# Performance work log

Hardware: AMD Instinct MI355X
Metric: run time of the kernel (lower is better)

Reference implementation:

```python
import jax, jax.numpy as jnp
import numpy as np

B = 256
N = 256


def setup_inputs() -> dict:
    key = jax.random.key(0)
    ks = jax.random.split(key, 6)
    X = jax.random.normal(ks[0], (B, N), dtype=jnp.float32)
    context = jax.random.normal(ks[1], (B, N), dtype=jnp.float32)
    W = jax.random.normal(ks[2], (N, N), dtype=jnp.float32) * 0.1
    scale = jnp.ones((1,), dtype=jnp.float32)
    A = jax.random.uniform(ks[3], (N, N), dtype=jnp.float32)
    cl_weight = jax.random.normal(ks[4], (N * N, N), dtype=jnp.float32) * 0.02
    cl_bias = jax.random.normal(ks[5], (N * N,), dtype=jnp.float32) * 0.02
    t = 3
    return {"X": X, "context": context, "W": W, "scale": scale, "A": A,
            "cl_weight": cl_weight, "cl_bias": cl_bias, "t": t}


def reference(X, context, W, scale, A, cl_weight, cl_bias, t):
    # context_L path: context-conditioned adjustment of W, shape [B, N, N]
    Bsz, n = X.shape
    adjust = (context @ cl_weight.T + cl_bias).reshape(Bsz, n, n)
    W_new = adjust + W  # broadcast [N,N] over batch
    # diag term: sum over rows i of (W_new @ A)[b, i, k] = einsum bij,jk->bk
    d = jnp.einsum('bij,jk->bk', W_new, A)
    eye = jnp.eye(n, dtype=X.dtype)
    L = d[:, :, None] * eye - W_new          # diag_embed(d) - W_new, [B,N,N]
    new_context = context * (t / (t + 1)) + X / (t + 1)
    L_T = scale * jnp.swapaxes(L, -1, -2)    # [B,N,N]
    update = jnp.einsum('bn,bnm->bm', X, L_T)  # matmul(X[...,None,:], L_T).squeeze()
    return (update, new_context)
```

## Files before the change

kernel.cpp:

```cpp
#include <hip/hip_runtime.h>

#define N 256
#define NN 65536

typedef __attribute__((ext_vector_type(8))) __bf16 bf16x8;
typedef __attribute__((ext_vector_type(4))) __bf16 bf16x4v;
typedef __attribute__((ext_vector_type(4))) float f32x4;

#define F_PART   0u
#define F_SPART  2097152u
#define F_WSC    2621440u
#define F_SFULL  2621696u
#define F_YADJ   2687232u
#define WS_FLOATS 2752768u

static __device__ __forceinline__ f32x4 mfma16(bf16x8 a, bf16x8 b, f32x4 c) {
  return __builtin_amdgcn_mfma_f32_16x16x32_bf16(a, b, c, 0, 0, 0);
}
static __device__ __forceinline__ bf16x4v pack4(float4 v) {
  bf16x4v r;
  r[0] = (__bf16)v.x; r[1] = (__bf16)v.y; r[2] = (__bf16)v.z; r[3] = (__bf16)v.w;
  return r;
}
static __device__ __forceinline__ bf16x8 pack8(float4 a, float4 b) {
  bf16x8 r;
  r[0] = (__bf16)a.x; r[1] = (__bf16)a.y; r[2] = (__bf16)a.z; r[3] = (__bf16)a.w;
  r[4] = (__bf16)b.x; r[5] = (__bf16)b.y; r[6] = (__bf16)b.z; r[7] = (__bf16)b.w;
  return r;
}

typedef __attribute__((address_space(1))) const unsigned int ga_u32;
typedef __attribute__((address_space(3))) unsigned int ls_u32;
static __device__ __forceinline__ void gload16(const void* g, void* l) {
  __builtin_amdgcn_global_load_lds((ga_u32*)g, (ls_u32*)l, 16, 0, 0);
}

#define BARV(NV)                                                          \
  asm volatile("s_waitcnt vmcnt(" #NV ") lgkmcnt(0)" ::: "memory");       \
  __builtin_amdgcn_s_barrier();                                           \
  __builtin_amdgcn_sched_barrier(0);
#define BARL()                                                            \
  asm volatile("s_waitcnt lgkmcnt(0)" ::: "memory");                      \
  __builtin_amdgcn_s_barrier();                                           \
  __builtin_amdgcn_sched_barrier(0);

__global__ void __launch_bounds__(256, 2) kbig(
    const float* __restrict__ X, const float* __restrict__ ctx,
    const float* __restrict__ W, const float* __restrict__ clb,
    const float* __restrict__ clw, float* __restrict__ ws)
{
  extern __shared__ char smem[];
  float* xl   = (float*)(smem + 65536);
  float* sred = (float*)(smem + 69632);
  float* red  = (float*)smem;
  const int t = threadIdx.x;
  const int bh = blockIdx.x >> 8;
  const int rem = blockIdx.x & 255;
  const int mt = rem >> 5, s = rem & 31;
  const int n0 = s * 8, m0g = mt * 32, b0g = bh * 128;

  const int lane = t & 63, w = t >> 6;
  const int wb = w * 32;
  const int l15 = lane & 15, lhi = lane >> 4;
  const int sw2 = (l15 & 7) << 4;

  bf16x8 af[2][8];
#pragma unroll
  for (int i = 0; i < 2; ++i)
#pragma unroll
    for (int c = 0; c < 8; ++c) {
      const float4* p = (const float4*)(ctx + (b0g + wb + i * 16 + l15) * N +
                                        c * 32 + lhi * 8);
      af[i][c] = pack8(p[0], p[1]);
    }
  if (t < 128) {
    const float4* xp = (const float4*)(X + (b0g + t) * N + n0);
    const float4 x0 = xp[0], x1 = xp[1];
    xl[0 * 128 + t] = x0.x; xl[1 * 128 + t] = x0.y;
    xl[2 * 128 + t] = x0.z; xl[3 * 128 + t] = x0.w;
    xl[4 * 128 + t] = x1.x; xl[5 * 128 + t] = x1.y;
    xl[6 * 128 + t] = x1.z; xl[7 * 128 + t] = x1.w;
  }
  __builtin_amdgcn_sched_barrier(0);

#define ISSUE_T(TT, BUFI)                                                   \
  {                                                                         \
    _Pragma("unroll")                                                       \
    for (int i = 0; i < 8; ++i) {                                           \
      const int rowl = w * 8 + i;                                           \
      const size_t grow = (size_t)((m0g + rowl) * 256 + n0 + (TT));         \
      gload16((const char*)clw + grow * 1024 +                              \
                  (size_t)((lane * 16) ^ ((rowl & 7) << 4)),                \
              smem + (BUFI) * 32768 + rowl * 1024);                         \
    }                                                                       \
  }

  const f32x4 zero = {0.f, 0.f, 0.f, 0.f};
  f32x4 acc[2][2];
  acc[0][0] = zero; acc[0][1] = zero; acc[1][0] = zero; acc[1][1] = zero;

#define COMP(NNV)                                                           \
  {                                                                         \
    const char* buf = smem + ((NNV) & 1) * 32768;                           \
    f32x4 h[2][2];                                                          \
    h[0][0] = zero; h[0][1] = zero; h[1][0] = zero; h[1][1] = zero;         \
    _Pragma("unroll")                                                       \
    for (int c = 0; c < 8; ++c) {                                           \
      const int colb = c * 128 + lhi * 32;                                  \
      const float4 p00 = *(const float4*)(buf + l15 * 1024 + (colb ^ sw2)); \
      const float4 p01 =                                                    \
          *(const float4*)(buf + l15 * 1024 + ((colb + 16) ^ sw2));         \
      const float4 p10 =                                                    \
          *(const float4*)(buf + (16 + l15) * 1024 + (colb ^ sw2));         \
      const float4 p11 =                                                    \
          *(const float4*)(buf + (16 + l15) * 1024 + ((colb + 16) ^ sw2));  \
      const bf16x8 b0 = pack8(p00, p01);                                    \
      const bf16x8 b1 = pack8(p10, p11);                                    \
      h[0][0] = mfma16(af[0][c], b0, h[0][0]);                              \
      h[0][1] = mfma16(af[0][c], b1, h[0][1]);                              \
      h[1][0] = mfma16(af[1][c], b0, h[1][0]);                              \
      h[1][1] = mfma16(af[1][c], b1, h[1][1]);                              \
    }                                                                       \
    _Pragma("unroll")                                                       \
    for (int fb = 0; fb < 2; ++fb) {                                        \
      _Pragma("unroll")                                                     \
      for (int r = 0; r < 4; ++r) {                                         \
        const int brow = wb + fb * 16 + lhi * 4 + r;                        \
        const float xv = xl[(NNV) * 128 + brow];                            \
        acc[fb][0][r] += xv * h[fb][0][r];                                  \
        acc[fb][1][r] += xv * h[fb][1][r];                                  \
        float v = h[fb][0][r] + h[fb][1][r];                                \
        v += __shfl_xor(v, 1); v += __shfl_xor(v, 2);                       \
        v += __shfl_xor(v, 4); v += __shfl_xor(v, 8);                       \
        if (l15 == 0) sred[(NNV) * 128 + brow] = v;                         \
      }                                                                     \
    }                                                                       \
  }

  ISSUE_T(0, 0) ISSUE_T(1, 1)
  BARV(8)
  COMP(0) BARL() ISSUE_T(2, 0)
  BARV(8)
  COMP(1) BARL() ISSUE_T(3, 1)
  BARV(8)
  COMP(2) BARL() ISSUE_T(4, 0)
  BARV(8)
  COMP(3) BARL() ISSUE_T(5, 1)
  BARV(8)
  COMP(4) BARL() ISSUE_T(6, 0)
  BARV(8)
  COMP(5) BARL() ISSUE_T(7, 1)
  BARV(8)
  COMP(6) BARL()
  BARV(0)
  COMP(7)
#undef ISSUE_T
#undef COMP

  const int base = blockIdx.x * 4096;
#pragma unroll
  for (int fb = 0; fb < 2; ++fb)
#pragma unroll
    for (int fm = 0; fm < 2; ++fm)
#pragma unroll
      for (int r = 0; r < 4; ++r)
        ws[F_PART + base + (wb + fb * 16 + lhi * 4 + r) * 32 + fm * 16 + l15] =
            acc[fb][fm][r];

  {
    const int bl = wb + (lane >> 1);
    const int nh = (lane & 1) * 4;
    float4 v;
    v.x = sred[(nh + 0) * 128 + bl];
    v.y = sred[(nh + 1) * 128 + bl];
    v.z = sred[(nh + 2) * 128 + bl];
    v.w = sred[(nh + 3) * 128 + bl];
    *(float4*)(ws + F_SPART + mt * NN + (b0g + bl) * N + n0 + nh) = v;
  }

  if (mt == 0 && bh == 0) {
    __syncthreads();
    const float4* wp = (const float4*)(W + t * N + s * 8);
    const float4* cp = (const float4*)(clb + t * N + s * 8);
    const float4 a0 = wp[0], a1 = wp[1], c0 = cp[0], c1 = cp[1];
    red[0 * 256 + t] = a0.x + c0.x; red[1 * 256 + t] = a0.y + c0.y;
    red[2 * 256 + t] = a0.z + c0.z; red[3 * 256 + t] = a0.w + c0.w;
    red[4 * 256 + t] = a1.x + c1.x; red[5 * 256 + t] = a1.y + c1.y;
    red[6 * 256 + t] = a1.z + c1.z; red[7 * 256 + t] = a1.w + c1.w;
    __syncthreads();
    if (t < 64) {
      const int jj = t >> 3, seg = t & 7;
      float v = 0.f;
#pragma unroll
      for (int i = 0; i < 32; ++i) v += red[jj * 256 + seg * 32 + i];
      v += __shfl_xor(v, 1);
      v += __shfl_xor(v, 2);
      v += __shfl_xor(v, 4);
      if (seg == 0) ws[F_WSC + s * 8 + jj] = v;
    }
  }
}

__global__ void __launch_bounds__(256) kred(float* __restrict__ ws)
{
  const int o = blockIdx.x * 256 + threadIdx.x;
  const int b = o >> 8, col = o & 255;
  const int mt = col >> 5, ml = col & 31;
  const int bhh = b >> 7, bl = b & 127;
  float y = 0.f;
#pragma unroll
  for (int si = 0; si < 32; ++si)
    y += ws[F_PART + (bhh * 256 + mt * 32 + si) * 4096 + bl * 32 + ml];
  ws[F_YADJ + o] = y;
  float sv = ws[F_WSC + col];
#pragma unroll
  for (int q = 0; q < 8; ++q)
    sv += ws[F_SPART + q * NN + o];
  ws[F_SFULL + o] = sv;
}

__global__ void __launch_bounds__(256) kfin(
    const float* __restrict__ X, const float* __restrict__ ctx,
    const float* __restrict__ W, const float* __restrict__ clb,
    const float* __restrict__ A, const float* __restrict__ scale,
    const int* __restrict__ tptr, float* __restrict__ out,
    float* __restrict__ ws)
{
  extern __shared__ char smem[];
  const int t = threadIdx.x, blk = blockIdx.x;
  const int b0 = (blk >> 3) * 32, k0 = (blk & 7) * 32;
  {
    const int row = t >> 3, q = t & 7;
    const int sw = (row & 7) << 4;
    const float4* sp = (const float4*)(ws + F_SFULL + (b0 + row) * N);
    const float4* xp = (const float4*)(X + (b0 + row) * N);
    const float4* wp = (const float4*)(W + (k0 + row) * N);
    const float4* cp = (const float4*)(clb + (k0 + row) * N);
#pragma unroll
    for (int i = 0; i < 8; ++i) {
      const int f4 = q * 8 + i;
      const int off = row * 512 + ((f4 * 8) ^ sw);
      *(bf16x4v*)(smem + off) = pack4(sp[f4]);
      *(bf16x4v*)(smem + 16384 + off) = pack4(xp[f4]);
      const float4 wv = wp[f4], cv = cp[f4];
      float4 s2;
      s2.x = wv.x + cv.x; s2.y = wv.y + cv.y;
      s2.z = wv.z + cv.z; s2.w = wv.w + cv.w;
      *(bf16x4v*)(smem + 49152 + off) = pack4(s2);
    }
    const float4* ap = (const float4*)(A + t * N + k0);
    char* at = smem + 32768;
#pragma unroll
    for (int i = 0; i < 8; ++i) {
      const float4 v = ap[i];
      const int kk = i * 4;
      *(__bf16*)(at + (kk + 0) * 512 + ((t * 2) ^ (((kk + 0) & 7) << 4))) = (__bf16)v.x;
      *(__bf16*)(at + (kk + 1) * 512 + ((t * 2) ^ (((kk + 1) & 7) << 4))) = (__bf16)v.y;
      *(__bf16*)(at + (kk + 2) * 512 + ((t * 2) ^ (((kk + 2) & 7) << 4))) = (__bf16)v.z;
      *(__bf16*)(at + (kk + 3) * 512 + ((t * 2) ^ (((kk + 3) & 7) << 4))) = (__bf16)v.w;
    }
  }
  __syncthreads();
  const int lane = t & 63, w = t >> 6;
  const int l15 = lane & 15, lhi = lane >> 4;
  const int wqb = (w >> 1) * 16, wqk = (w & 1) * 16;
  const int swz = (l15 & 7) << 4;
  f32x4 accd = {0.f, 0.f, 0.f, 0.f}, accw = {0.f, 0.f, 0.f, 0.f};
#pragma unroll
  for (int c = 0; c < 8; ++c) {
    const int kb = c * 64 + lhi * 16;
    bf16x8 as  = *(const bf16x8*)(smem + (wqb + l15) * 512 + (kb ^ swz));
    bf16x8 aat = *(const bf16x8*)(smem + 32768 + (wqk + l15) * 512 + (kb ^ swz));
    bf16x8 ax  = *(const bf16x8*)(smem + 16384 + (wqb + l15) * 512 + (kb ^ swz));
    bf16x8 awc = *(const bf16x8*)(smem + 49152 + (wqk + l15) * 512 + (kb ^ swz));
    accd = mfma16(as, aat, accd);
    accw = mfma16(ax, awc, accw);
  }
  const float sc = scale[0];
  const float tf = (float)(*tptr);
  const float c1 = tf / (tf + 1.f), c2 = 1.f / (tf + 1.f);
#pragma unroll
  for (int r = 0; r < 4; ++r) {
    const int b = b0 + wqb + lhi * 4 + r, k = k0 + wqk + l15;
    const int idx = b * N + k;
    const float xv = X[idx];
    out[idx] = sc * (xv * accd[r] - accw[r] - ws[F_YADJ + idx]);
    out[NN + idx] = ctx[idx] * c1 + xv * c2;
  }
}

extern "C" void kernel_launch(void* const* d_in, const int* in_sizes, int n_in,
                              void* d_out, int out_size, void* d_ws, size_t ws_size,
                              hipStream_t stream)
{
  (void)in_sizes; (void)n_in; (void)out_size;
  const float* X     = (const float*)d_in[0];
  const float* ctx   = (const float*)d_in[1];
  const float* W     = (const float*)d_in[2];
  const float* scale = (const float*)d_in[3];
  const float* A     = (const float*)d_in[4];
  const float* clw   = (const float*)d_in[5];
  const float* clb   = (const float*)d_in[6];
  const int*   tptr  = (const int*)d_in[7];
  float* out = (float*)d_out;
  float* ws  = (float*)d_ws;

  if (ws_size < (size_t)WS_FLOATS * sizeof(float)) return;

  (void)hipFuncSetAttribute((const void*)kbig,
                            hipFuncAttributeMaxDynamicSharedMemorySize, 73728);
  (void)hipFuncSetAttribute((const void*)kfin,
                            hipFuncAttributeMaxDynamicSharedMemorySize, 65536);

  kbig<<<512, 256, 73728, stream>>>(X, ctx, W, clb, clw, ws);
  kred<<<256, 256, 0, stream>>>(ws);
  kfin<<<64, 256, 65536, stream>>>(X, ctx, W, clb, A, scale, tptr, out, ws);
}
```

Baseline: 58.94 us.

## Stage cl_weight through registers as bf16 in a triple-buffered LDS ring

The direct global-to-LDS fp32 loads of cl_weight are replaced by register loads that are converted to bf16 before being written to LDS, using a three-slot ring of 16 KB buffers. This halves the LDS footprint and the LDS read traffic, and lets the MFMA loop read packed bf16 operands without converting them. The cost is extra VGPRs for two in-flight register batches, extra conversion work on the load path, and the loss of the asynchronous global_load_lds path, which may expose global latency. Dynamic shared memory per block drops from 72 KB to 56 KB.

Result: faster. 53.07 us (-10.0%).

```diff
diff --git a/kernel.cpp b/kernel.cpp
--- a/kernel.cpp
+++ b/kernel.cpp
@@ -29,16 +29,6 @@
   return r;
 }
 
-typedef __attribute__((address_space(1))) const unsigned int ga_u32;
-typedef __attribute__((address_space(3))) unsigned int ls_u32;
-static __device__ __forceinline__ void gload16(const void* g, void* l) {
-  __builtin_amdgcn_global_load_lds((ga_u32*)g, (ls_u32*)l, 16, 0, 0);
-}
-
-#define BARV(NV)                                                          \
-  asm volatile("s_waitcnt vmcnt(" #NV ") lgkmcnt(0)" ::: "memory");       \
-  __builtin_amdgcn_s_barrier();                                           \
-  __builtin_amdgcn_sched_barrier(0);
 #define BARL()                                                            \
   asm volatile("s_waitcnt lgkmcnt(0)" ::: "memory");                      \
   __builtin_amdgcn_s_barrier();                                           \
@@ -50,8 +40,8 @@
     const float* __restrict__ clw, float* __restrict__ ws)
 {
   extern __shared__ char smem[];
-  float* xl   = (float*)(smem + 65536);
-  float* sred = (float*)(smem + 69632);
+  float* xl   = (float*)(smem + 49152);
+  float* sred = (float*)(smem + 53248);
   float* red  = (float*)smem;
   const int t = threadIdx.x;
   const int bh = blockIdx.x >> 8;
@@ -62,7 +52,8 @@
   const int lane = t & 63, w = t >> 6;
   const int wb = w * 32;
   const int l15 = lane & 15, lhi = lane >> 4;
-  const int sw2 = (l15 & 7) << 4;
+  const int swz = (l15 & 7) << 4;
+  const float4* clwf4 = (const float4*)clw;
 
   bf16x8 af[2][8];
 #pragma unroll
@@ -81,19 +72,25 @@
     xl[4 * 128 + t] = x1.x; xl[5 * 128 + t] = x1.y;
     xl[6 * 128 + t] = x1.z; xl[7 * 128 + t] = x1.w;
   }
+
+#define ISSUE(TT, R)                                                        \
+  _Pragma("unroll")                                                         \
+  for (int i = 0; i < 8; ++i) {                                             \
+    const int rowl = w * 8 + i;                                             \
+    R[i] = clwf4[(size_t)((m0g + rowl) * 256 + n0 + (TT)) * 64 + lane];     \
+  }
+#define WRITE(TT, R)                                                        \
+  _Pragma("unroll")                                                         \
+  for (int i = 0; i < 8; ++i) {                                             \
+    const int rowl = w * 8 + i;                                             \
+    *(bf16x4v*)(smem + ((TT) % 3) * 16384 + rowl * 512 +                    \
+                ((lane * 8) ^ ((rowl & 7) << 4))) = pack4(R[i]);            \
+  }
+
+  float4 rA[8], rB[8];
+  ISSUE(0, rA)
+  ISSUE(1, rB)
   __builtin_amdgcn_sched_barrier(0);
-
-#define ISSUE_T(TT, BUFI)                                                   \
-  {                                                                         \
-    _Pragma("unroll")                                                       \
-    for (int i = 0; i < 8; ++i) {                                           \
-      const int rowl = w * 8 + i;                                           \
-      const size_t grow = (size_t)((m0g + rowl) * 256 + n0 + (TT));         \
-      gload16((const char*)clw + grow * 1024 +                              \
-                  (size_t)((lane * 16) ^ ((rowl & 7) << 4)),                \
-              smem + (BUFI) * 32768 + rowl * 1024);                         \
-    }                                                                       \
-  }
 
   const f32x4 zero = {0.f, 0.f, 0.f, 0.f};
   f32x4 acc[2][2];
@@ -101,21 +98,14 @@
 
 #define COMP(NNV)                                                           \
   {                                                                         \
-    const char* buf = smem + ((NNV) & 1) * 32768;                           \
+    const char* buf = smem + ((NNV) % 3) * 16384;                           \
     f32x4 h[2][2];                                                          \
     h[0][0] = zero; h[0][1] = zero; h[1][0] = zero; h[1][1] = zero;         \
     _Pragma("unroll")                                                       \
     for (int c = 0; c < 8; ++c) {                                           \
-      const int colb = c * 128 + lhi * 32;                                  \
-      const float4 p00 = *(const float4*)(buf + l15 * 1024 + (colb ^ sw2)); \
-      const float4 p01 =                                                    \
-          *(const float4*)(buf + l15 * 1024 + ((colb + 16) ^ sw2));         \
-      const float4 p10 =                                                    \
-          *(const float4*)(buf + (16 + l15) * 1024 + (colb ^ sw2));         \
-      const float4 p11 =                                                    \
-          *(const float4*)(buf + (16 + l15) * 1024 + ((colb + 16) ^ sw2));  \
-      const bf16x8 b0 = pack8(p00, p01);                                    \
-      const bf16x8 b1 = pack8(p10, p11);                                    \
+      const int kb = c * 64 + lhi * 16;                                     \
+      bf16x8 b0 = *(const bf16x8*)(buf + l15 * 512 + (kb ^ swz));           \
+      bf16x8 b1 = *(const bf16x8*)(buf + (16 + l15) * 512 + (kb ^ swz));    \
       h[0][0] = mfma16(af[0][c], b0, h[0][0]);                              \
       h[0][1] = mfma16(af[0][c], b1, h[0][1]);                              \
       h[1][0] = mfma16(af[1][c], b0, h[1][0]);                              \
@@ -137,24 +127,18 @@
     }                                                                       \
   }
 
-  ISSUE_T(0, 0) ISSUE_T(1, 1)
-  BARV(8)
-  COMP(0) BARL() ISSUE_T(2, 0)
-  BARV(8)
-  COMP(1) BARL() ISSUE_T(3, 1)
-  BARV(8)
-  COMP(2) BARL() ISSUE_T(4, 0)
-  BARV(8)
-  COMP(3) BARL() ISSUE_T(5, 1)
-  BARV(8)
-  COMP(4) BARL() ISSUE_T(6, 0)
-  BARV(8)
-  COMP(5) BARL() ISSUE_T(7, 1)
-  BARV(8)
-  COMP(6) BARL()
-  BARV(0)
+  WRITE(0, rA)
+  BARL();
+  ISSUE(2, rA) __builtin_amdgcn_sched_barrier(0); WRITE(1, rB) BARL(); COMP(0)
+  ISSUE(3, rB) __builtin_amdgcn_sched_barrier(0); WRITE(2, rA) BARL(); COMP(1)
+  ISSUE(4, rA) __builtin_amdgcn_sched_barrier(0); WRITE(3, rB) BARL(); COMP(2)
+  ISSUE(5, rB) __builtin_amdgcn_sched_barrier(0); WRITE(4, rA) BARL(); COMP(3)
+  ISSUE(6, rA) __builtin_amdgcn_sched_barrier(0); WRITE(5, rB) BARL(); COMP(4)
+  ISSUE(7, rB) __builtin_amdgcn_sched_barrier(0); WRITE(6, rA) BARL(); COMP(5)
+  WRITE(7, rB) BARL(); COMP(6)
   COMP(7)
-#undef ISSUE_T
+#undef ISSUE
+#undef WRITE
 #undef COMP
 
   const int base = blockIdx.x * 4096;
@@ -308,11 +292,11 @@
   if (ws_size < (size_t)WS_FLOATS * sizeof(float)) return;
 
   (void)hipFuncSetAttribute((const void*)kbig,
-                            hipFuncAttributeMaxDynamicSharedMemorySize, 73728);
+                            hipFuncAttributeMaxDynamicSharedMemorySize, 57344);
   (void)hipFuncSetAttribute((const void*)kfin,
                             hipFuncAttributeMaxDynamicSharedMemorySize, 65536);
 
-  kbig<<<512, 256, 73728, stream>>>(X, ctx, W, clb, clw, ws);
+  kbig<<<512, 256, 57344, stream>>>(X, ctx, W, clb, clw, ws);
   kred<<<256, 256, 0, stream>>>(ws);
   kfin<<<64, 256, 65536, stream>>>(X, ctx, W, clb, A, scale, tptr, out, ws);
 }
```
